# Kernel optimization log

Measured on AMD Instinct MI355X. Metric: run time of the kernel, lower is better.

## Reference

```python
import jax, jax.numpy as jnp
import numpy as np

S, R, CM, CZ, C, H = 128, 256, 256, 128, 32, 8
EPS = 1e-5


def layer_norm(x, w, b):
    mu = jnp.mean(x, axis=-1, keepdims=True)
    var = jnp.mean(jnp.square(x - mu), axis=-1, keepdims=True)
    return (x - mu) * jax.lax.rsqrt(var + EPS) * w + b


def setup_inputs() -> dict:
    key = jax.random.key(0)
    ks = jax.random.split(key, 10)
    s = 0.02
    return {
        "m": jax.random.normal(ks[0], (S, R, CM), jnp.float32),
        "z": jax.random.normal(ks[1], (R, R, CZ), jnp.float32),
        "ln_m_w": jnp.ones((CM,), jnp.float32),
        "ln_m_b": jnp.zeros((CM,), jnp.float32),
        "ln_z_w": jnp.ones((CZ,), jnp.float32),
        "ln_z_b": jnp.zeros((CZ,), jnp.float32),
        "Wz": jax.random.normal(ks[2], (CZ, H), jnp.float32) * s,
        "Wq": jax.random.normal(ks[3], (CM, H * C), jnp.float32) * s,
        "Wk": jax.random.normal(ks[4], (CM, H * C), jnp.float32) * s,
        "Wv": jax.random.normal(ks[5], (CM, H * C), jnp.float32) * s,
        "Wg": jax.random.normal(ks[6], (CM, H * C), jnp.float32) * s,
        "bg": jnp.ones((H * C,), jnp.float32),
        "Wo": jax.random.normal(ks[7], (H * C, CM), jnp.float32) * s,
        "bo": jnp.zeros((CM,), jnp.float32),
    }


def reference(m, z, ln_m_w, ln_m_b, ln_z_w, ln_z_b, Wz, Wq, Wk, Wv, Wg, bg, Wo, bo):
    mn = layer_norm(m, ln_m_w, ln_m_b)              # [S,R,CM]
    zn = layer_norm(z, ln_z_w, ln_z_b)              # [R,R,CZ]
    bias = jnp.einsum('qkz,zh->hqk', zn, Wz)        # [H,R,R] pair bias
    q = (mn @ Wq).reshape(S, R, H, C) * (C ** -0.5)
    k = (mn @ Wk).reshape(S, R, H, C)
    v = (mn @ Wv).reshape(S, R, H, C)
    logits = jnp.einsum('sqhc,skhc->shqk', q, k) + bias[None]  # [S,H,R,R]
    a = jax.nn.softmax(logits, axis=-1)
    o = jnp.einsum('shqk,skhc->sqhc', a, v)         # [S,R,H,C]
    g = jax.nn.sigmoid(mn @ Wg + bg).reshape(S, R, H, C)
    return (g * o).reshape(S, R, H * C) @ Wo + bo   # [S,R,CM]
```

## Files before the change

### kernel.cpp

```cpp
#include <hip/hip_runtime.h>
#include <math.h>

#define S_DIM 128
#define R_DIM 256
#define CM_DIM 256
#define CZ_DIM 128
#define C_DIM 32
#define H_DIM 8
#define HC_DIM 256
#define LN_EPS 1e-5f
#define ZPAD 132
#define HSZ 1048576
#define BIAS_SCALE 16384.0f
#define BIAS_INV (1.0f / 16384.0f)

typedef _Float16 half8 __attribute__((ext_vector_type(8)));
typedef _Float16 half4 __attribute__((ext_vector_type(4)));
typedef float f32x4 __attribute__((ext_vector_type(4)));
typedef short short4v __attribute__((ext_vector_type(4)));
typedef short short8v __attribute__((ext_vector_type(8)));

__device__ __forceinline__ float wave_sum(float v) {
#pragma unroll
    for (int off = 32; off > 0; off >>= 1) v += __shfl_down(v, off);
    return v;
}

__device__ __forceinline__ void gload16(const _Float16* src, _Float16* dst) {
    __builtin_amdgcn_global_load_lds((const __attribute__((address_space(1))) void*)src,
                                     (__attribute__((address_space(3))) void*)dst, 16, 0, 0);
}

__global__ __launch_bounds__(256) void convert_w_kernel(const float* __restrict__ Wq,
                                                        const float* __restrict__ Wk,
                                                        const float* __restrict__ Wv,
                                                        const float* __restrict__ Wg,
                                                        const float* __restrict__ Wo,
                                                        _Float16* __restrict__ w3) {
    int kb = blockIdx.x;
    int mat = blockIdx.y;
    const float* src = (mat == 0) ? Wq : (mat == 1) ? Wk : (mat == 2) ? Wv : (mat == 3) ? Wg : Wo;
    int n = threadIdx.x;
    _Float16 tmp[32];
#pragma unroll
    for (int kk = 0; kk < 32; kk++)
        tmp[kk] = (_Float16)src[(size_t)(kb * 32 + kk) * 256 + n];
    half8* dst = (half8*)(w3 + (size_t)mat * 65536 + (size_t)kb * 8192 + (size_t)n * 32);
#pragma unroll
    for (int i = 0; i < 4; i++) dst[i] = *(half8*)&tmp[i * 8];
}

__global__ __launch_bounds__(64) void prep_wz_kernel(const float* __restrict__ w,
                                                     const float* __restrict__ b,
                                                     const float* __restrict__ Wz,
                                                     float* __restrict__ u_g,
                                                     float* __restrict__ UB) {
    int lane = threadIdx.x;
    float w0 = w[lane], w1 = w[lane + 64];
    float b0 = b[lane], b1 = b[lane + 64];
#pragma unroll
    for (int h = 0; h < H_DIM; h++) {
        float wz0 = Wz[lane * H_DIM + h], wz1 = Wz[(lane + 64) * H_DIM + h];
        float u0 = w0 * wz0, u1 = w1 * wz1;
        u_g[h * ZPAD + lane] = u0;
        u_g[h * ZPAD + lane + 64] = u1;
        float U = wave_sum(u0 + u1);
        float B = wave_sum(b0 * wz0 + b1 * wz1);
        if (lane == 0) { UB[h] = U; UB[8 + h] = B; }
    }
}

__global__ __launch_bounds__(64) void ln_m_kernel(const float* __restrict__ m,
                                                  const float* __restrict__ w,
                                                  const float* __restrict__ b,
                                                  _Float16* __restrict__ mn) {
    int row = blockIdx.x;
    int t = threadIdx.x;
    const float4* mrow = (const float4*)(m + (size_t)row * CM_DIM);
    float4 x = mrow[t];
    float s = x.x + x.y + x.z + x.w;
    float ss = x.x * x.x + x.y * x.y + x.z * x.z + x.w * x.w;
    s = wave_sum(s);
    ss = wave_sum(ss);
    s = __shfl(s, 0);
    ss = __shfl(ss, 0);
    float mean = s * (1.0f / CM_DIM);
    float var = ss * (1.0f / CM_DIM) - mean * mean;
    float rsig = rsqrtf(var + LN_EPS);
    float4 wv = ((const float4*)w)[t];
    float4 bv = ((const float4*)b)[t];
    half4 o;
    o[0] = (_Float16)((x.x - mean) * rsig * wv.x + bv.x);
    o[1] = (_Float16)((x.y - mean) * rsig * wv.y + bv.y);
    o[2] = (_Float16)((x.z - mean) * rsig * wv.z + bv.z);
    o[3] = (_Float16)((x.w - mean) * rsig * wv.w + bv.w);
    *(half4*)(mn + (size_t)row * CM_DIM + t * 4) = o;
}

__global__ __launch_bounds__(256) void ln_z_bias_kernel(const float* __restrict__ z,
                                                        const float* __restrict__ u_g,
                                                        const float* __restrict__ UB,
                                                        short* __restrict__ bias_i) {
    __shared__ __align__(16) float zt[64 * ZPAD];
    __shared__ __align__(16) float ut[8 * ZPAD];
    __shared__ float UBs[16];
    int tid = threadIdx.x;
    int row0 = blockIdx.x * 64;
    for (int i = tid; i < 8 * ZPAD; i += 256) ut[i] = u_g[i];
    if (tid < 16) UBs[tid] = UB[tid];
    const float4* zsrc = (const float4*)(z + (size_t)row0 * CZ_DIM);
#pragma unroll
    for (int i = 0; i < 8; i++) {
        int idx = tid + i * 256;
        float4 v = zsrc[idx];
        int r = idx >> 5, c4 = (idx & 31) * 4;
        *(float4*)&zt[r * ZPAD + c4] = v;
    }
    __syncthreads();
    int r = tid >> 2, p = tid & 3;
    const float* zr = &zt[r * ZPAD];
    const float* u0p = &ut[p * ZPAD];
    const float* u1p = &ut[(p + 4) * ZPAD];
    float s = 0.f, ss = 0.f, a0 = 0.f, a1 = 0.f;
#pragma unroll
    for (int c = 0; c < CZ_DIM; c += 4) {
        float4 x = *(const float4*)&zr[c];
        float4 uu0 = *(const float4*)&u0p[c];
        float4 uu1 = *(const float4*)&u1p[c];
        s += x.x + x.y + x.z + x.w;
        ss += x.x * x.x + x.y * x.y + x.z * x.z + x.w * x.w;
        a0 += x.x * uu0.x + x.y * uu0.y + x.z * uu0.z + x.w * uu0.w;
        a1 += x.x * uu1.x + x.y * uu1.y + x.z * uu1.z + x.w * uu1.w;
    }
    float mu = s * (1.0f / CZ_DIM);
    float var = ss * (1.0f / CZ_DIM) - mu * mu;
    float rsig = rsqrtf(var + LN_EPS);
    int row = row0 + r;
    float b0v = rsig * (a0 - mu * UBs[p]) + UBs[8 + p];
    float b1v = rsig * (a1 - mu * UBs[4 + p]) + UBs[12 + p];
    int i0 = (int)rintf(b0v * BIAS_SCALE);
    int i1 = (int)rintf(b1v * BIAS_SCALE);
    i0 = i0 > 32767 ? 32767 : (i0 < -32768 ? -32768 : i0);
    i1 = i1 > 32767 ? 32767 : (i1 < -32768 ? -32768 : i1);
    bias_i[(size_t)p * 65536 + row] = (short)i0;
    bias_i[(size_t)(p + 4) * 65536 + row] = (short)i1;
}

__global__ __launch_bounds__(256, 3) void proj_mfma_kernel(const _Float16* __restrict__ A,
                                                           const _Float16* __restrict__ w3,
                                                           const float* __restrict__ bg,
                                                           _Float16* __restrict__ qh,
                                                           _Float16* __restrict__ kh,
                                                           _Float16* __restrict__ vh,
                                                           _Float16* __restrict__ gh) {
    __shared__ _Float16 As[64 * 256];
    __shared__ _Float16 Os[64 * 132];
    int m0 = blockIdx.x * 64;
    int col0 = blockIdx.y * 128;
    int tid = threadIdx.x, lane = tid & 63, wave = tid >> 6;
    int lrow = lane & 15, g = lane >> 4, lk8 = g * 8;
    int wr = wave >> 1, wc = wave & 1;

#pragma unroll
    for (int i = 0; i < 8; i++) {
        int row = i * 8 + (tid >> 5);
        int c = (tid & 31) ^ (row & 7);
        gload16(A + (size_t)(m0 + row) * 256 + c * 8, As + (size_t)(i * 256 + tid) * 8);
    }
    __syncthreads();

    const float qscale = 0.17677669529663687f;
    const _Float16* Wlane = w3 + (size_t)(col0 + wc * 64 + lrow) * 32 + lk8;
    for (int mat = 0; mat < 4; mat++) {
        f32x4 acc[2][4];
#pragma unroll
        for (int i = 0; i < 2; i++)
#pragma unroll
            for (int j = 0; j < 4; j++) acc[i][j] = (f32x4){0.f, 0.f, 0.f, 0.f};
#pragma unroll
        for (int hf = 0; hf < 2; hf++) {
            half8 breg[4][4];
#pragma unroll
            for (int kq = 0; kq < 4; kq++)
#pragma unroll
                for (int nf = 0; nf < 4; nf++)
                    breg[kq][nf] = *(const half8*)(Wlane + (size_t)mat * 65536 +
                                                   (size_t)(hf * 4 + kq) * 8192 + nf * 512);
#pragma unroll
            for (int kq = 0; kq < 4; kq++) {
                int kb = hf * 4 + kq;
                half8 af[2];
#pragma unroll
                for (int mf = 0; mf < 2; mf++) {
                    int row = wr * 32 + mf * 16 + lrow;
                    af[mf] = *(half8*)&As[row * 256 + (((kb * 4 + g) ^ (row & 7)) * 8)];
                }
#pragma unroll
                for (int mf = 0; mf < 2; mf++)
#pragma unroll
                    for (int nf = 0; nf < 4; nf++)
                        acc[mf][nf] = __builtin_amdgcn_mfma_f32_16x16x32_f16(af[mf], breg[kq][nf],
                                                                             acc[mf][nf], 0, 0, 0);
            }
        }
        __syncthreads();
#pragma unroll
        for (int mf = 0; mf < 2; mf++)
#pragma unroll
            for (int nf = 0; nf < 4; nf++)
#pragma unroll
                for (int ri = 0; ri < 4; ri++) {
                    int srow = wr * 32 + mf * 16 + g * 4 + ri;
                    int scol = wc * 64 + nf * 16 + lrow;
                    float v = acc[mf][nf][ri];
                    if (mat == 0) v *= qscale;
                    if (mat == 3) v = 1.0f / (1.0f + __expf(-(v + bg[col0 + scol])));
                    Os[srow * 132 + scol] = (_Float16)v;
                }
        __syncthreads();
        if (mat < 3) {
            _Float16* Out = (mat == 0) ? qh : (mat == 1) ? kh : vh;
#pragma unroll
            for (int j = 0; j < 4; j++) {
                int hh = (col0 >> 5) + j;
                int row = tid >> 2, cOff = (tid & 3) * 8;
                half8 v8 = *(half8*)&Os[row * 132 + j * 32 + cOff];
                *(half8*)(Out + (size_t)hh * HSZ + (size_t)(m0 + row) * 32 + cOff) = v8;
            }
        } else {
#pragma unroll
            for (int i = 0; i < 4; i++) {
                int c2 = tid + i * 256;
                int row = c2 >> 4, cOff = (c2 & 15) * 8;
                half8 v8 = *(half8*)&Os[row * 132 + cOff];
                *(half8*)(gh + (size_t)(m0 + row) * 256 + col0 + cOff) = v8;
            }
        }
    }
}

__global__ __launch_bounds__(512, 1) void attn_mfma_kernel(const _Float16* __restrict__ qh,
                                                           const _Float16* __restrict__ kh,
                                                           const _Float16* __restrict__ vh,
                                                           const _Float16* __restrict__ gh,
                                                           const short* __restrict__ bias_i,
                                                           _Float16* __restrict__ oh) {
    __shared__ short bias_s[256][264];
    __shared__ _Float16 K_s[64][40];
    __shared__ _Float16 VT_s[32][72];
    int h = blockIdx.x, sg = blockIdx.y;
    int tid = threadIdx.x;
    int lane = tid & 63, wave = tid >> 6;
    int lrow = lane & 15, g = lane >> 4, lk8 = g * 8;
    int qw = wave * 32;

    const short* bsrc = bias_i + (size_t)h * 65536;
#pragma unroll
    for (int i = 0; i < 16; i++) {
        int e = (tid + i * 512) * 8;
        short8v v = *(const short8v*)(bsrc + e);
        *(short8v*)&bias_s[e >> 8][e & 255] = v;
    }

    const _Float16* qbase = qh + (size_t)h * HSZ;
    const _Float16* kbase = kh + (size_t)h * HSZ;
    const _Float16* vbase = vh + (size_t)h * HSZ;
    _Float16* obase = oh + (size_t)h * HSZ;

    bool isK = (wave < 4);
    int key = (tid & 255) >> 2, koff = (tid & 3) * 8;
    int vkey = tid & 63, vc0 = ((tid >> 6) & 3) * 8;

    for (int si = 0; si < 4; si++) {
        int s = sg * 4 + si;
        half8 qfr[2];
#pragma unroll
        for (int qf = 0; qf < 2; qf++)
            qfr[qf] = *(const half8*)(qbase + (size_t)(s * 256 + qw + qf * 16 + lrow) * 32 + lk8);

        f32x4 oaccT[2][2];
        float m_run[2], l_run[2];
#pragma unroll
        for (int qf = 0; qf < 2; qf++) {
            oaccT[qf][0] = (f32x4){0.f, 0.f, 0.f, 0.f};
            oaccT[qf][1] = (f32x4){0.f, 0.f, 0.f, 0.f};
            m_run[qf] = -1e30f;
            l_run[qf] = 0.f;
        }

        half8 stg;
        if (isK) stg = *(const half8*)(kbase + (size_t)(s * 256 + key) * 32 + koff);
        else     stg = *(const half8*)(vbase + (size_t)(s * 256 + vkey) * 32 + vc0);

        for (int kb = 0; kb < 4; kb++) {
            __syncthreads();
            if (isK) {
                *(half8*)&K_s[key][koff] = stg;
            } else {
#pragma unroll
                for (int j = 0; j < 8; j++) VT_s[vc0 + j][vkey] = stg[j];
            }
            if (kb < 3) {
                int nk = (kb + 1) * 64;
                if (isK) stg = *(const half8*)(kbase + (size_t)(s * 256 + nk + key) * 32 + koff);
                else     stg = *(const half8*)(vbase + (size_t)(s * 256 + nk + vkey) * 32 + vc0);
            }
            __syncthreads();

            half8 kfr[4];
#pragma unroll
            for (int kf = 0; kf < 4; kf++) kfr[kf] = *(half8*)&K_s[kf * 16 + lrow][lk8];

#pragma unroll
            for (int qf = 0; qf < 2; qf++) {
                f32x4 sf[4];
#pragma unroll
                for (int kf = 0; kf < 4; kf++) {
                    f32x4 zero = (f32x4){0.f, 0.f, 0.f, 0.f};
                    sf[kf] = __builtin_amdgcn_mfma_f32_16x16x32_f16(kfr[kf], qfr[qf], zero, 0, 0, 0);
                }
                int q = qw + qf * 16 + lrow;
#pragma unroll
                for (int kf = 0; kf < 4; kf++) {
                    short4v bh = *(short4v*)&bias_s[q][kb * 64 + kf * 16 + 4 * g];
#pragma unroll
                    for (int ri = 0; ri < 4; ri++) sf[kf][ri] += (float)bh[ri] * BIAS_INV;
                }
                float tm = -1e30f;
#pragma unroll
                for (int kf = 0; kf < 4; kf++)
#pragma unroll
                    for (int ri = 0; ri < 4; ri++) tm = fmaxf(tm, sf[kf][ri]);
                tm = fmaxf(tm, __shfl_xor(tm, 16));
                tm = fmaxf(tm, __shfl_xor(tm, 32));
                float nm = fmaxf(m_run[qf], tm);
                float sc = __expf(m_run[qf] - nm);
                m_run[qf] = nm;
                oaccT[qf][0] *= sc;
                oaccT[qf][1] *= sc;
                float p[4][4];
                float rs = 0.f;
#pragma unroll
                for (int kf = 0; kf < 4; kf++)
#pragma unroll
                    for (int ri = 0; ri < 4; ri++) {
                        float pv = __expf(sf[kf][ri] - nm);
                        p[kf][ri] = pv;
                        rs += pv;
                    }
                rs += __shfl_xor(rs, 16);
                rs += __shfl_xor(rs, 32);
                l_run[qf] = l_run[qf] * sc + rs;
                unsigned w8[8];
#pragma unroll
                for (int kf = 0; kf < 4; kf++)
#pragma unroll
                    for (int t = 0; t < 2; t++) {
                        union { _Float16 hh[2]; unsigned u; } pk;
                        pk.hh[0] = (_Float16)p[kf][2 * t];
                        pk.hh[1] = (_Float16)p[kf][2 * t + 1];
                        w8[2 * kf + t] = pk.u;
                    }
#pragma unroll
                for (int ks = 0; ks < 2; ks++) {
                    union { unsigned u[4]; half8 h8; } pb;
#pragma unroll
                    for (int u = 0; u < 4; u++) {
                        int srcl = ((g & 1) * 2 + (u >> 1)) * 16 + lrow;
                        unsigned lo_sh = (unsigned)__shfl((int)w8[4 * ks + (u & 1)], srcl);
                        unsigned hi_sh = (unsigned)__shfl((int)w8[4 * ks + (u & 1) + 2], srcl);
                        pb.u[u] = (g >> 1) ? hi_sh : lo_sh;
                    }
#pragma unroll
                    for (int cf = 0; cf < 2; cf++) {
                        half8 va = *(half8*)&VT_s[cf * 16 + lrow][ks * 32 + lk8];
                        oaccT[qf][cf] =
                            __builtin_amdgcn_mfma_f32_16x16x32_f16(va, pb.h8, oaccT[qf][cf], 0, 0, 0);
                    }
                }
            }
        }
#pragma unroll
        for (int qf = 0; qf < 2; qf++) {
            float inv = 1.0f / l_run[qf];
            int q = qw + qf * 16 + lrow;
#pragma unroll
            for (int cf = 0; cf < 2; cf++) {
                half4 gv4 = *(const half4*)(gh + (size_t)(s * 256 + q) * 256 + h * 32 + cf * 16 + 4 * g);
                half4 o4;
#pragma unroll
                for (int ri = 0; ri < 4; ri++)
                    o4[ri] = (_Float16)(oaccT[qf][cf][ri] * inv * (float)gv4[ri]);
                *(half4*)(obase + (size_t)(s * 256 + q) * 32 + cf * 16 + 4 * g) = o4;
            }
        }
    }
}

__global__ __launch_bounds__(256, 4) void out_mfma_kernel(const _Float16* __restrict__ oh,
                                                          const _Float16* __restrict__ w3o,
                                                          const float* __restrict__ bo,
                                                          float* __restrict__ out) {
    __shared__ _Float16 As[64 * 256];
    int m0 = blockIdx.x * 64;
    int col0 = blockIdx.y * 128;
    int tid = threadIdx.x, lane = tid & 63, wave = tid >> 6;
    int lrow = lane & 15, g = lane >> 4, lk8 = g * 8;
    int wr = wave >> 1, wc = wave & 1;

#pragma unroll
    for (int i = 0; i < 8; i++) {
        int row = i * 8 + (tid >> 5);
        int cc = (tid & 31) ^ (row & 7);
        gload16(oh + (size_t)(cc >> 2) * HSZ + (size_t)(m0 + row) * 32 + (cc & 3) * 8,
                As + (size_t)(i * 256 + tid) * 8);
    }
    __syncthreads();

    const _Float16* Wlane = w3o + (size_t)(col0 + wc * 64 + lrow) * 32 + lk8;
    f32x4 acc[2][4];
#pragma unroll
    for (int i = 0; i < 2; i++)
#pragma unroll
        for (int j = 0; j < 4; j++) acc[i][j] = (f32x4){0.f, 0.f, 0.f, 0.f};
#pragma unroll
    for (int hf = 0; hf < 2; hf++) {
        half8 breg[4][4];
#pragma unroll
        for (int kq = 0; kq < 4; kq++)
#pragma unroll
            for (int nf = 0; nf < 4; nf++)
                breg[kq][nf] = *(const half8*)(Wlane + (size_t)(hf * 4 + kq) * 8192 + nf * 512);
#pragma unroll
        for (int kq = 0; kq < 4; kq++) {
            int kb = hf * 4 + kq;
            half8 af[2];
#pragma unroll
            for (int mf = 0; mf < 2; mf++) {
                int row = wr * 32 + mf * 16 + lrow;
                af[mf] = *(half8*)&As[row * 256 + (((kb * 4 + g) ^ (row & 7)) * 8)];
            }
#pragma unroll
            for (int mf = 0; mf < 2; mf++)
#pragma unroll
                for (int nf = 0; nf < 4; nf++)
                    acc[mf][nf] = __builtin_amdgcn_mfma_f32_16x16x32_f16(af[mf], breg[kq][nf],
                                                                         acc[mf][nf], 0, 0, 0);
        }
    }
#pragma unroll
    for (int mf = 0; mf < 2; mf++)
#pragma unroll
        for (int nf = 0; nf < 4; nf++)
#pragma unroll
            for (int ri = 0; ri < 4; ri++) {
                int row = m0 + wr * 32 + mf * 16 + g * 4 + ri;
                int col = col0 + wc * 64 + nf * 16 + lrow;
                out[(size_t)row * 256 + col] = acc[mf][nf][ri] + bo[col];
            }
}

extern "C" void kernel_launch(void* const* d_in, const int* in_sizes, int n_in,
                              void* d_out, int out_size, void* d_ws, size_t ws_size,
                              hipStream_t stream) {
    const float* m = (const float*)d_in[0];
    const float* z = (const float*)d_in[1];
    const float* ln_m_w = (const float*)d_in[2];
    const float* ln_m_b = (const float*)d_in[3];
    const float* ln_z_w = (const float*)d_in[4];
    const float* ln_z_b = (const float*)d_in[5];
    const float* Wz = (const float*)d_in[6];
    const float* Wq = (const float*)d_in[7];
    const float* Wk = (const float*)d_in[8];
    const float* Wv = (const float*)d_in[9];
    const float* Wg = (const float*)d_in[10];
    const float* bg = (const float*)d_in[11];
    const float* Wo = (const float*)d_in[12];
    const float* bo = (const float*)d_in[13];
    float* out = (float*)d_out;

    const size_t NE = (size_t)S_DIM * R_DIM * CM_DIM;
    _Float16* hb = (_Float16*)d_ws;
    _Float16* mn_h = hb;
    _Float16* qh = hb + NE;
    _Float16* kh = hb + 2 * NE;
    _Float16* vh = hb + 3 * NE;
    _Float16* gh = hb + 4 * NE;
    _Float16* oh = hb + 5 * NE;
    _Float16* w3 = hb + 6 * NE;
    float* u_g = (float*)(hb + 6 * NE + 5 * 65536);
    float* UB = u_g + 8 * ZPAD;
    short* bias_i = (short*)(UB + 16);

    hipLaunchKernelGGL(convert_w_kernel, dim3(8, 5), dim3(256), 0, stream,
                       Wq, Wk, Wv, Wg, Wo, w3);
    hipLaunchKernelGGL(prep_wz_kernel, dim3(1), dim3(64), 0, stream,
                       ln_z_w, ln_z_b, Wz, u_g, UB);
    hipLaunchKernelGGL(ln_m_kernel, dim3(S_DIM * R_DIM), dim3(64), 0, stream,
                       m, ln_m_w, ln_m_b, mn_h);
    hipLaunchKernelGGL(ln_z_bias_kernel, dim3(1024), dim3(256), 0, stream,
                       z, u_g, UB, bias_i);
    hipLaunchKernelGGL(proj_mfma_kernel, dim3(512, 2), dim3(256), 0, stream,
                       mn_h, w3, bg, qh, kh, vh, gh);
    hipLaunchKernelGGL(attn_mfma_kernel, dim3(H_DIM, 32), dim3(512), 0, stream,
                       qh, kh, vh, gh, bias_i, oh);
    hipLaunchKernelGGL(out_mfma_kernel, dim3(512, 2), dim3(256), 0, stream,
                       oh, w3 + 4 * 65536, bo, out);
}
```

Measured before the change: 138.1 us.

## Keep A fragments in registers and double-buffer weight tiles through LDS

In both the projection and output GEMM kernels, the A tile now goes straight from global memory into per-wave registers instead of through shared memory. The B (weight) tiles are staged into a swizzled, double-buffered LDS ring with async loads, prefetched two steps ahead. This replaces per-lane direct global weight loads with cooperative coalesced LDS staging, aiming to overlap weight fetch with MFMA and cut redundant global traffic. In exchange it adds barriers per K-step and raises register pressure from holding 16 half8 A fragments per lane.

```diff
diff --git a/kernel.cpp b/kernel.cpp
--- a/kernel.cpp
+++ b/kernel.cpp
@@ -153,90 +153,107 @@
                                                            _Float16* __restrict__ kh,
                                                            _Float16* __restrict__ vh,
                                                            _Float16* __restrict__ gh) {
-    __shared__ _Float16 As[64 * 256];
+    __shared__ _Float16 Bs[2][64 * 128];
     __shared__ _Float16 Os[64 * 132];
     int m0 = blockIdx.x * 64;
     int col0 = blockIdx.y * 128;
     int tid = threadIdx.x, lane = tid & 63, wave = tid >> 6;
-    int lrow = lane & 15, g = lane >> 4, lk8 = g * 8;
+    int lrow = lane & 15, g = lane >> 4;
     int wr = wave >> 1, wc = wave & 1;
-
-#pragma unroll
-    for (int i = 0; i < 8; i++) {
-        int row = i * 8 + (tid >> 5);
-        int c = (tid & 31) ^ (row & 7);
-        gload16(A + (size_t)(m0 + row) * 256 + c * 8, As + (size_t)(i * 256 + tid) * 8);
-    }
+    const float qscale = 0.17677669529663687f;
+
+    half8 afr[2][8];
+#pragma unroll
+    for (int mf = 0; mf < 2; mf++)
+#pragma unroll
+        for (int kb = 0; kb < 8; kb++)
+            afr[mf][kb] = *(const half8*)(A + (size_t)(m0 + wr * 32 + mf * 16 + lrow) * 256 +
+                                          kb * 32 + g * 8);
+
+#define STAGE_B(T, BUF)                                                              \
+    {                                                                                \
+        int mat_ = (T) >> 2, kp_ = (T) & 3;                                          \
+        _Float16* dst_ = &Bs[BUF][0];                                                \
+        const _Float16* src_ = w3 + (size_t)mat_ * 65536 + (size_t)kp_ * 16384;      \
+        _Pragma("unroll") for (int i_ = 0; i_ < 4; i_++) {                           \
+            int j_ = tid + i_ * 256;                                                 \
+            int n_ = j_ >> 3, cL_ = j_ & 7;                                          \
+            int c_ = cL_ ^ (n_ & 7);                                                 \
+            int kbL_ = c_ >> 2, q_ = c_ & 3;                                         \
+            gload16(src_ + (size_t)kbL_ * 8192 + (size_t)(col0 + n_) * 32 + q_ * 8,  \
+                    dst_ + (size_t)j_ * 8);                                          \
+        }                                                                            \
+    }
+
+    STAGE_B(0, 0);
+    STAGE_B(1, 1);
     __syncthreads();
 
-    const float qscale = 0.17677669529663687f;
-    const _Float16* Wlane = w3 + (size_t)(col0 + wc * 64 + lrow) * 32 + lk8;
-    for (int mat = 0; mat < 4; mat++) {
-        f32x4 acc[2][4];
-#pragma unroll
-        for (int i = 0; i < 2; i++)
-#pragma unroll
-            for (int j = 0; j < 4; j++) acc[i][j] = (f32x4){0.f, 0.f, 0.f, 0.f};
-#pragma unroll
-        for (int hf = 0; hf < 2; hf++) {
-            half8 breg[4][4];
-#pragma unroll
-            for (int kq = 0; kq < 4; kq++)
+    f32x4 acc[2][4];
+    for (int t = 0; t < 16; t++) {
+        int buf = t & 1;
+        int mat = t >> 2, kp = t & 3;
+        if (kp == 0) {
+#pragma unroll
+            for (int i = 0; i < 2; i++)
+#pragma unroll
+                for (int j = 0; j < 4; j++) acc[i][j] = (f32x4){0.f, 0.f, 0.f, 0.f};
+        }
+#pragma unroll
+        for (int kbL = 0; kbL < 2; kbL++) {
+            int kb = kp * 2 + kbL;
+            half8 bf[4];
+#pragma unroll
+            for (int nf = 0; nf < 4; nf++) {
+                int col = wc * 64 + nf * 16 + lrow;
+                int chunk = (kbL * 4 + g) ^ (col & 7);
+                bf[nf] = *(half8*)&Bs[buf][(size_t)(col * 8 + chunk) * 8];
+            }
+#pragma unroll
+            for (int mf = 0; mf < 2; mf++)
 #pragma unroll
                 for (int nf = 0; nf < 4; nf++)
-                    breg[kq][nf] = *(const half8*)(Wlane + (size_t)mat * 65536 +
-                                                   (size_t)(hf * 4 + kq) * 8192 + nf * 512);
-#pragma unroll
-            for (int kq = 0; kq < 4; kq++) {
-                int kb = hf * 4 + kq;
-                half8 af[2];
-#pragma unroll
-                for (int mf = 0; mf < 2; mf++) {
-                    int row = wr * 32 + mf * 16 + lrow;
-                    af[mf] = *(half8*)&As[row * 256 + (((kb * 4 + g) ^ (row & 7)) * 8)];
+                    acc[mf][nf] = __builtin_amdgcn_mfma_f32_16x16x32_f16(afr[mf][kb], bf[nf],
+                                                                         acc[mf][nf], 0, 0, 0);
+        }
+        if (kp == 3) {
+#pragma unroll
+            for (int mf = 0; mf < 2; mf++)
+#pragma unroll
+                for (int nf = 0; nf < 4; nf++)
+#pragma unroll
+                    for (int ri = 0; ri < 4; ri++) {
+                        int srow = wr * 32 + mf * 16 + g * 4 + ri;
+                        int scol = wc * 64 + nf * 16 + lrow;
+                        float v = acc[mf][nf][ri];
+                        if (mat == 0) v *= qscale;
+                        if (mat == 3) v = 1.0f / (1.0f + __expf(-(v + bg[col0 + scol])));
+                        Os[srow * 132 + scol] = (_Float16)v;
+                    }
+            __syncthreads();
+            if (mat < 3) {
+                _Float16* Out = (mat == 0) ? qh : (mat == 1) ? kh : vh;
+#pragma unroll
+                for (int j = 0; j < 4; j++) {
+                    int hh = (col0 >> 5) + j;
+                    int row = tid >> 2, cOff = (tid & 3) * 8;
+                    half8 v8 = *(half8*)&Os[row * 132 + j * 32 + cOff];
+                    *(half8*)(Out + (size_t)hh * HSZ + (size_t)(m0 + row) * 32 + cOff) = v8;
                 }
-#pragma unroll
-                for (int mf = 0; mf < 2; mf++)
-#pragma unroll
-                    for (int nf = 0; nf < 4; nf++)
-                        acc[mf][nf] = __builtin_amdgcn_mfma_f32_16x16x32_f16(af[mf], breg[kq][nf],
-                                                                             acc[mf][nf], 0, 0, 0);
+            } else {
+#pragma unroll
+                for (int i = 0; i < 4; i++) {
+                    int c2 = tid + i * 256;
+                    int row = c2 >> 4, cOff = (c2 & 15) * 8;
+                    half8 v8 = *(half8*)&Os[row * 132 + cOff];
+                    *(half8*)(gh + (size_t)(m0 + row) * 256 + col0 + cOff) = v8;
+                }
             }
         }
         __syncthreads();
-#pragma unroll
-        for (int mf = 0; mf < 2; mf++)
-#pragma unroll
-            for (int nf = 0; nf < 4; nf++)
-#pragma unroll
-                for (int ri = 0; ri < 4; ri++) {
-                    int srow = wr * 32 + mf * 16 + g * 4 + ri;
-                    int scol = wc * 64 + nf * 16 + lrow;
-                    float v = acc[mf][nf][ri];
-                    if (mat == 0) v *= qscale;
-                    if (mat == 3) v = 1.0f / (1.0f + __expf(-(v + bg[col0 + scol])));
-                    Os[srow * 132 + scol] = (_Float16)v;
-                }
-        __syncthreads();
-        if (mat < 3) {
-            _Float16* Out = (mat == 0) ? qh : (mat == 1) ? kh : vh;
-#pragma unroll
-            for (int j = 0; j < 4; j++) {
-                int hh = (col0 >> 5) + j;
-                int row = tid >> 2, cOff = (tid & 3) * 8;
-                half8 v8 = *(half8*)&Os[row * 132 + j * 32 + cOff];
-                *(half8*)(Out + (size_t)hh * HSZ + (size_t)(m0 + row) * 32 + cOff) = v8;
-            }
-        } else {
-#pragma unroll
-            for (int i = 0; i < 4; i++) {
-                int c2 = tid + i * 256;
-                int row = c2 >> 4, cOff = (c2 & 15) * 8;
-                half8 v8 = *(half8*)&Os[row * 132 + cOff];
-                *(half8*)(gh + (size_t)(m0 + row) * 256 + col0 + cOff) = v8;
-            }
-        }
-    }
+        if (t + 2 < 16) STAGE_B(t + 2, buf);
+    }
+#undef STAGE_B
 }
 
 __global__ __launch_bounds__(512, 1) void attn_mfma_kernel(const _Float16* __restrict__ qh,
@@ -401,53 +418,70 @@
                                                           const _Float16* __restrict__ w3o,
                                                           const float* __restrict__ bo,
                                                           float* __restrict__ out) {
-    __shared__ _Float16 As[64 * 256];
+    __shared__ _Float16 Bs[2][64 * 128];
     int m0 = blockIdx.x * 64;
     int col0 = blockIdx.y * 128;
     int tid = threadIdx.x, lane = tid & 63, wave = tid >> 6;
-    int lrow = lane & 15, g = lane >> 4, lk8 = g * 8;
+    int lrow = lane & 15, g = lane >> 4;
     int wr = wave >> 1, wc = wave & 1;
 
-#pragma unroll
-    for (int i = 0; i < 8; i++) {
-        int row = i * 8 + (tid >> 5);
-        int cc = (tid & 31) ^ (row & 7);
-        gload16(oh + (size_t)(cc >> 2) * HSZ + (size_t)(m0 + row) * 32 + (cc & 3) * 8,
-                As + (size_t)(i * 256 + tid) * 8);
-    }
+    half8 afr[2][8];
+#pragma unroll
+    for (int mf = 0; mf < 2; mf++)
+#pragma unroll
+        for (int kb = 0; kb < 8; kb++)
+            afr[mf][kb] = *(const half8*)(oh + (size_t)kb * HSZ +
+                                          (size_t)(m0 + wr * 32 + mf * 16 + lrow) * 32 + g * 8);
+
+#define STAGE_BO(T, BUF)                                                             \
+    {                                                                                \
+        int kp_ = (T);                                                               \
+        _Float16* dst_ = &Bs[BUF][0];                                                \
+        const _Float16* src_ = w3o + (size_t)kp_ * 16384;                            \
+        _Pragma("unroll") for (int i_ = 0; i_ < 4; i_++) {                           \
+            int j_ = tid + i_ * 256;                                                 \
+            int n_ = j_ >> 3, cL_ = j_ & 7;                                          \
+            int c_ = cL_ ^ (n_ & 7);                                                 \
+            int kbL_ = c_ >> 2, q_ = c_ & 3;                                         \
+            gload16(src_ + (size_t)kbL_ * 8192 + (size_t)(col0 + n_) * 32 + q_ * 8,  \
+                    dst_ + (size_t)j_ * 8);                                          \
+        }                                                                            \
+    }
+
+    STAGE_BO(0, 0);
+    STAGE_BO(1, 1);
     __syncthreads();
 
-    const _Float16* Wlane = w3o + (size_t)(col0 + wc * 64 + lrow) * 32 + lk8;
     f32x4 acc[2][4];
 #pragma unroll
     for (int i = 0; i < 2; i++)
 #pragma unroll
         for (int j = 0; j < 4; j++) acc[i][j] = (f32x4){0.f, 0.f, 0.f, 0.f};
-#pragma unroll
-    for (int hf = 0; hf < 2; hf++) {
-        half8 breg[4][4];
-#pragma unroll
-        for (int kq = 0; kq < 4; kq++)
-#pragma unroll
-            for (int nf = 0; nf < 4; nf++)
-                breg[kq][nf] = *(const half8*)(Wlane + (size_t)(hf * 4 + kq) * 8192 + nf * 512);
-#pragma unroll
-        for (int kq = 0; kq < 4; kq++) {
-            int kb = hf * 4 + kq;
-            half8 af[2];
-#pragma unroll
-            for (int mf = 0; mf < 2; mf++) {
-                int row = wr * 32 + mf * 16 + lrow;
-                af[mf] = *(half8*)&As[row * 256 + (((kb * 4 + g) ^ (row & 7)) * 8)];
+
+    for (int t = 0; t < 4; t++) {
+        int buf = t & 1;
+#pragma unroll
+        for (int kbL = 0; kbL < 2; kbL++) {
+            int kb = t * 2 + kbL;
+            half8 bf[4];
+#pragma unroll
+            for (int nf = 0; nf < 4; nf++) {
+                int col = wc * 64 + nf * 16 + lrow;
+                int chunk = (kbL * 4 + g) ^ (col & 7);
+                bf[nf] = *(half8*)&Bs[buf][(size_t)(col * 8 + chunk) * 8];
             }
 #pragma unroll
             for (int mf = 0; mf < 2; mf++)
 #pragma unroll
                 for (int nf = 0; nf < 4; nf++)
-                    acc[mf][nf] = __builtin_amdgcn_mfma_f32_16x16x32_f16(af[mf], breg[kq][nf],
+                    acc[mf][nf] = __builtin_amdgcn_mfma_f32_16x16x32_f16(afr[mf][kb], bf[nf],
                                                                          acc[mf][nf], 0, 0, 0);
         }
-    }
+        __syncthreads();
+        if (t + 2 < 4) STAGE_BO(t + 2, buf);
+    }
+#undef STAGE_BO
+
 #pragma unroll
     for (int mf = 0; mf < 2; mf++)
 #pragma unroll
```

After: 126.3 us. -8.5%, faster.
